# Optimization experiments

Measured on AMD Instinct MI355X. Metric: run time of the kernel, lower is better.

Reference implementation:

```python
import jax, jax.numpy as jnp
import numpy as np

VOCAB, XS, HS, NCLASS = 32000, 256, 256, 2
B, DEPTH = 128, 9
NTREE = 2 ** (DEPTH + 1) - 1  # 1023 nodes per perfect binary tree


def setup_inputs() -> dict:
    key = jax.random.key(0)
    ks = jax.random.split(key, 10)
    return {
        'types1': jax.random.randint(ks[0], (B, NTREE), 0, VOCAB, dtype=jnp.int32),
        'types2': jax.random.randint(ks[1], (B, NTREE), 0, VOCAB, dtype=jnp.int32),
        'emb': jax.random.normal(ks[2], (VOCAB, XS), jnp.float32) * 0.1,
        'W_iou': jax.random.normal(ks[3], (3 * HS, XS), jnp.float32) * 0.05,
        'U_iou': jax.random.normal(ks[4], (3 * HS, HS), jnp.float32) * 0.05,
        'b_iou': jnp.zeros((1, 3 * HS), jnp.float32),
        'U_f_w': jax.random.normal(ks[5], (HS, HS), jnp.float32) * 0.05,
        'U_f_b': jnp.zeros((HS,), jnp.float32),
        'cls_w': jax.random.normal(ks[6], (NCLASS, HS), jnp.float32) * 0.05,
        'cls_b': jnp.zeros((NCLASS,), jnp.float32),
    }


def _tree_forward(types, emb, W_iou, U_iou, b_iou, U_f_w, U_f_b):
    # types: [B, NTREE] heap layout (node j has children 2j+1, 2j+2)
    x = emb[types]                       # [B, N, XS] embedding gather
    wx = x @ W_iou.T                     # [B, N, 3H] leaf iou (DGL reduce overwrites it for internal nodes)
    h = jnp.zeros((types.shape[0], NTREE, HS), wx.dtype)
    c = jnp.zeros_like(h)
    for lvl in range(DEPTH, -1, -1):     # bottom-up topological levels (static)
        idx = np.arange(2 ** lvl - 1, 2 ** (lvl + 1) - 1)
        if lvl == DEPTH:  # leaves: no mailbox, keep W_iou(x)
            iou = wx[:, idx] + b_iou
            c_sum = 0.0
        else:
            ch = np.stack([2 * idx + 1, 2 * idx + 2], axis=-1)  # [n, 2]
            h_ch = h[:, ch]              # [B, n, 2, H] child mailbox
            c_ch = c[:, ch]
            h_tild = h_ch.sum(axis=2)
            f = jax.nn.sigmoid(h_ch @ U_f_w.T + U_f_b)
            c_sum = (f * c_ch).sum(axis=2)
            iou = h_tild @ U_iou.T + b_iou  # overwrites wx per DGL semantics
        i, o, u = jnp.split(iou, 3, axis=-1)
        c_new = jax.nn.sigmoid(i) * jnp.tanh(u) + c_sum
        h_new = jax.nn.sigmoid(o) * jnp.tanh(c_new)
        h = h.at[:, idx].set(h_new)
        c = c.at[:, idx].set(c_new)
    return h.mean(axis=1)                # AvgPooling over nodes -> [B, H]


def reference(types1, types2, emb, W_iou, U_iou, b_iou, U_f_w, U_f_b, cls_w, cls_b):
    rep1 = _tree_forward(types1, emb, W_iou, U_iou, b_iou, U_f_w, U_f_b)
    rep2 = _tree_forward(types2, emb, W_iou, U_iou, b_iou, U_f_w, U_f_b)
    return jnp.abs(rep1 - rep2) @ cls_w.T + cls_b  # [B, NCLASS]
```

## Files before the change

kernel.cpp:

```cpp
#include <hip/hip_runtime.h>
#include <math.h>


typedef _Float16 h16;
typedef h16 f16x8 __attribute__((ext_vector_type(8)));
typedef h16 h16x4 __attribute__((ext_vector_type(4)));
typedef float f32x4 __attribute__((ext_vector_type(4)));

#define HS 256
#define NTREE 1023
#define B2 256

#define DMA16(gp, lp) __builtin_amdgcn_global_load_lds( \
    (const __attribute__((address_space(1))) void*)(gp), \
    (__attribute__((address_space(3))) void*)(lp), 16, 0, 0)

__device__ __forceinline__ float sigf(float x){
  return __builtin_amdgcn_rcpf(1.0f + exp2f(x * -1.44269504f));
}
__device__ __forceinline__ float sig_mul_tanh(float a, float b){
  const float E1 = exp2f(a * -1.44269504f);
  const float E2 = exp2f(fminf(b * -2.88539008f, 126.0f));
  return (1.0f - E2) * __builtin_amdgcn_rcpf((1.0f + E1) * (1.0f + E2));
}

__global__ __launch_bounds__(256) void convert_all(const float* __restrict__ emb,
    const float* __restrict__ Ufw, const float* __restrict__ Uiou,
    const float* __restrict__ Wiou, h16* __restrict__ emb16,
    h16* __restrict__ W16, h16* __restrict__ Wx16, float* __restrict__ rep){
  if (blockIdx.x < 64)
    ((float4*)rep)[blockIdx.x*256 + threadIdx.x] = make_float4(0.f,0.f,0.f,0.f);
  const size_t i0 = ((size_t)blockIdx.x*256 + threadIdx.x)*8;
  const float* src; h16* dst; size_t off;
  if (i0 < 8192000UL){ src = emb;  dst = emb16;       off = i0; }
  else if (i0 < 8257536UL){ src = Ufw;  dst = W16;        off = i0 - 8192000UL; }
  else if (i0 < 8454144UL){ src = Uiou; dst = W16+65536;  off = i0 - 8257536UL; }
  else               { src = Wiou; dst = Wx16;       off = i0 - 8454144UL; }
  const float4 v0 = *(const float4*)&src[off];
  const float4 v1 = *(const float4*)&src[off+4];
  f16x8 o;
  o[0]=(h16)v0.x; o[1]=(h16)v0.y; o[2]=(h16)v0.z; o[3]=(h16)v0.w;
  o[4]=(h16)v1.x; o[5]=(h16)v1.y; o[6]=(h16)v1.z; o[7]=(h16)v1.w;
  *(f16x8*)&dst[off] = o;
}

__global__ __launch_bounds__(256) void swizzle_all(const h16* __restrict__ W16,
    const h16* __restrict__ Wx16, h16* __restrict__ Wfrag,
    h16* __restrict__ WxFrag){
  const int tid = blockIdx.x*256 + threadIdx.x;
  if (tid < 65536){
    const int lane = tid & 63;
    const int f    = (tid >> 6) & 15;
    const int kc   = (tid >> 10) & 7;
    const int cb   = tid >> 13;
    const int g = f >> 2, cf = f & 3;
    const int row = g*256 + cb*64 + cf*16 + (lane & 15);
    const int col = kc*32 + (lane >> 4)*8;
    const f16x8 v = *(const f16x8*)&W16[(size_t)row*256 + col];
    *(f16x8*)&Wfrag[(size_t)tid*8] = v;
  } else {
    const int t2 = tid - 65536;
    const int lane = t2 & 63;
    const int frag = t2 >> 6;
    const int cb  = frag / 96;
    const int rem = frag % 96;
    const int kc  = rem / 12;
    const int f   = rem % 12;
    const int g = f >> 2, cf = f & 3;
    const int row = g*256 + cb*64 + cf*16 + (lane & 15);
    const int col = kc*32 + (lane >> 4)*8;
    const f16x8 v = *(const f16x8*)&Wx16[(size_t)row*256 + col];
    *(f16x8*)&WxFrag[(size_t)frag*512 + lane*8] = v;
  }
}

__global__ __launch_bounds__(256,3) void ht_mfma(const h16* __restrict__ emb16,
    const h16* __restrict__ WxFrag, const float* __restrict__ biou,
    h16* __restrict__ hT, h16* __restrict__ cT){
  __shared__ h16 ldsA[4*8*64*8];
  __shared__ h16 ldsB[12*64*8];
  const int t = threadIdx.x, w = t >> 6, l = t & 63;
  const int q = l >> 4, li = l & 15;
  const int waveR = w & 1, waveC = w >> 1;
  const int bx = blockIdx.x;

  {
    const int grow = bx*64 + w*16 + li;
    const size_t abase = (size_t)grow * 256;
    #pragma unroll
    for (int kc=0; kc<8; ++kc)
      DMA16(emb16 + abase + kc*32 + q*8, &ldsA[(w*8 + kc)*512]);
  }

  for (int cb=0; cb<4; ++cb){
    const h16* wfBase = WxFrag + (size_t)cb*8*12*512 + (size_t)l*8;

    #pragma unroll
    for (int i=0; i<3; ++i)
      DMA16(wfBase + ((size_t)(w*3 + i))*512, &ldsB[(w*3 + i)*512]);
    __syncthreads();

    f32x4 acc[3][2][2] = {};
    #pragma unroll
    for (int kc=0; kc<8; ++kc){
      f16x8 aF[2], bF[3][2];
      #pragma unroll
      for (int rt=0; rt<2; ++rt)
        aF[rt] = *(const f16x8*)&ldsA[(((waveR*2 + rt)*8 + kc)*64 + l)*8];
      #pragma unroll
      for (int g=0; g<3; ++g)
        #pragma unroll
        for (int ct=0; ct<2; ++ct)
          bF[g][ct] = *(const f16x8*)&ldsB[((g*4 + waveC*2 + ct)*64 + l)*8];
      __syncthreads();
      if (kc < 7){
        #pragma unroll
        for (int i=0; i<3; ++i)
          DMA16(wfBase + ((size_t)(kc+1)*12 + w*3 + i)*512,
                &ldsB[(w*3 + i)*512]);
      }
      #pragma unroll
      for (int g=0; g<3; ++g)
        #pragma unroll
        for (int rt=0; rt<2; ++rt)
          #pragma unroll
          for (int ct=0; ct<2; ++ct)
            acc[g][rt][ct] = __builtin_amdgcn_mfma_f32_16x16x32_f16(
                aF[rt], bF[g][ct], acc[g][rt][ct], 0,0,0);
      __syncthreads();
    }

    #pragma unroll
    for (int ct=0; ct<2; ++ct){
      const int c = cb*64 + waveC*32 + ct*16 + li;
      const float bi = biou[c], bo = biou[256+c], bu = biou[512+c];
      #pragma unroll
      for (int rt=0; rt<2; ++rt){
        #pragma unroll
        for (int reg=0; reg<4; ++reg){
          const int row = bx*64 + waveR*32 + rt*16 + q*4 + reg;
          const float iv = acc[0][rt][ct][reg] + bi;
          const float ov = acc[1][rt][ct][reg] + bo;
          const float uv = acc[2][rt][ct][reg] + bu;
          const float cc = sig_mul_tanh(iv, uv);
          const float hh = sig_mul_tanh(ov, cc);
          hT[(size_t)row*256 + c] = (h16)hh;
          cT[(size_t)row*256 + c] = (h16)cc;
        }
      }
    }
  }
}

__global__ __launch_bounds__(256,3) void gt16_mfma(const h16* __restrict__ hT,
    const h16* __restrict__ Wfrag, const float* __restrict__ biou,
    const float* __restrict__ Ufb, h16* __restrict__ GT16){
  __shared__ h16 ldsA[4*8*64*8];
  __shared__ h16 ldsB[16*64*8];
  const int t = threadIdx.x, w = t >> 6, l = t & 63;
  const int q = l >> 4, li = l & 15;
  const int waveR = w & 1, waveC = w >> 1;
  const int bx = blockIdx.x;

  {
    const int grow = bx*64 + w*16 + li;
    const size_t abase = (size_t)grow * 256;
    #pragma unroll
    for (int kc=0; kc<8; ++kc)
      DMA16(hT + abase + kc*32 + q*8, &ldsA[(w*8 + kc)*512]);
  }

  for (int cb=0; cb<4; ++cb){
    const h16* wfBase = Wfrag + (size_t)cb*8*16*512 + (size_t)l*8;

    #pragma unroll
    for (int i=0; i<4; ++i)
      DMA16(wfBase + ((size_t)(w*4 + i))*512, &ldsB[(w*4 + i)*512]);
    __syncthreads();

    f32x4 acc[4][2][2] = {};
    #pragma unroll
    for (int kc=0; kc<8; ++kc){
      f16x8 aF[2], bF[4][2];
      #pragma unroll
      for (int rt=0; rt<2; ++rt)
        aF[rt] = *(const f16x8*)&ldsA[(((waveR*2 + rt)*8 + kc)*64 + l)*8];
      #pragma unroll
      for (int g=0; g<4; ++g)
        #pragma unroll
        for (int ct=0; ct<2; ++ct)
          bF[g][ct] = *(const f16x8*)&ldsB[((g*4 + waveC*2 + ct)*64 + l)*8];
      __syncthreads();
      if (kc < 7){
        #pragma unroll
        for (int i=0; i<4; ++i)
          DMA16(wfBase + ((size_t)(kc+1)*16 + w*4 + i)*512,
                &ldsB[(w*4 + i)*512]);
      }
      #pragma unroll
      for (int g=0; g<4; ++g)
        #pragma unroll
        for (int rt=0; rt<2; ++rt)
          #pragma unroll
          for (int ct=0; ct<2; ++ct)
            acc[g][rt][ct] = __builtin_amdgcn_mfma_f32_16x16x32_f16(
                aF[rt], bF[g][ct], acc[g][rt][ct], 0,0,0);
      __syncthreads();
    }

    #pragma unroll
    for (int ct=0; ct<2; ++ct){
      const int c = cb*64 + waveC*32 + ct*16 + li;
      const float fb  = Ufb[c];
      const float bi2 = 0.5f*biou[c], bo2 = 0.5f*biou[256+c], bu2 = 0.5f*biou[512+c];
      #pragma unroll
      for (int rt=0; rt<2; ++rt){
        #pragma unroll
        for (int reg=0; reg<4; ++reg){
          const int row = bx*64 + waveR*32 + rt*16 + q*4 + reg;
          h16x4 o;
          o[0] = (h16)(acc[0][rt][ct][reg] + fb);
          o[1] = (h16)(acc[1][rt][ct][reg] + bi2);
          o[2] = (h16)(acc[2][rt][ct][reg] + bo2);
          o[3] = (h16)(acc[3][rt][ct][reg] + bu2);
          *(h16x4*)&GT16[(size_t)row*1024 + c*4] = o;
        }
      }
    }
  }
}

__global__ __launch_bounds__(256) void lvl8_cell(const int* __restrict__ t1,
    const int* __restrict__ t2, const h16* __restrict__ GT16,
    const h16* __restrict__ cT, const h16* __restrict__ hT,
    h16* __restrict__ hUpHigh, h16* __restrict__ cPar,
    float* __restrict__ rep){
  const int k = threadIdx.x;
  const int m0 = blockIdx.x*32;
  const int rr = m0 >> 8;
  const int* tp = (rr < 128) ? t1 : t2;
  const int b = rr & 127;
  float s = 0.f;
  #pragma unroll 4
  for (int p=0; p<32; ++p){
    const int m = m0 + p, jn = m & 255;
    const size_t vl = (size_t)tp[b*NTREE + 511 + 2*jn];
    const size_t vr = (size_t)tp[b*NTREE + 512 + 2*jn];
    const h16x4 gl = *(const h16x4*)&GT16[vl*1024 + k*4];
    const h16x4 gr = *(const h16x4*)&GT16[vr*1024 + k*4];
    const float cl = (float)cT[vl*256 + k];
    const float cr = (float)cT[vr*256 + k];
    const float fl = sigf((float)gl[0]);
    const float fr = sigf((float)gr[0]);
    const float iv = (float)gl[1] + (float)gr[1];
    const float ov = (float)gl[2] + (float)gr[2];
    const float uv = (float)gl[3] + (float)gr[3];
    const float cnew = sig_mul_tanh(iv, uv) + fl*cl + fr*cr;
    const float hnew = sig_mul_tanh(ov, cnew);
    hUpHigh[((size_t)jn*256 + rr)*256 + k] = (h16)hnew;
    cPar[(size_t)m*256 + k] = (h16)cnew;
    s += (float)hT[vl*256 + k] + (float)hT[vr*256 + k];
  }
  atomicAdd(&rep[rr*HS + k], s);
}

__global__ __launch_bounds__(256,3) void level_mfma(
    const h16* __restrict__ hChild, const h16* __restrict__ cChild,
    const h16* __restrict__ Wfrag,
    const float* __restrict__ biou, const float* __restrict__ Ufb,
    h16* __restrict__ hUpW, h16* __restrict__ cPar,
    int log2n, int cbN, int cOff, int ndOff){
  const int n = 1 << log2n;
  const int mask2 = 2*n - 1;
  __shared__ h16 ldsA[4*8*64*8];
  __shared__ h16 ldsB[16*64*8];
  const int t = threadIdx.x, w = t >> 6, l = t & 63;
  const int q = l >> 4, li = l & 15;
  const int waveR = w & 1, waveC = w >> 1;
  const int bx = blockIdx.x;

  {
    const int grow = bx*64 + w*16 + li;
    const int cidx = grow & mask2;
    const int rr   = grow >> (log2n + 1);
    const size_t abase = ((size_t)(cOff + cidx)*256 + rr)*256;
    #pragma unroll
    for (int kc=0; kc<8; ++kc)
      DMA16(hChild + abase + kc*32 + q*8, &ldsA[(w*8 + kc)*512]);
  }

  for (int cb=0; cb<cbN; ++cb){
    const int cbi = blockIdx.y*cbN + cb;
    const int colBase = cbi*64;
    const h16* wfBase = Wfrag + (size_t)cbi*8*16*512 + (size_t)l*8;

    #pragma unroll
    for (int i=0; i<4; ++i)
      DMA16(wfBase + ((size_t)(w*4 + i))*512, &ldsB[(w*4 + i)*512]);
    __syncthreads();

    f32x4 acc[4][2][2] = {};
    #pragma unroll
    for (int kc=0; kc<8; ++kc){
      f16x8 aF[2], bF[4][2];
      #pragma unroll
      for (int rt=0; rt<2; ++rt)
        aF[rt] = *(const f16x8*)&ldsA[(((waveR*2 + rt)*8 + kc)*64 + l)*8];
      #pragma unroll
      for (int g=0; g<4; ++g)
        #pragma unroll
        for (int ct=0; ct<2; ++ct)
          bF[g][ct] = *(const f16x8*)&ldsB[((g*4 + waveC*2 + ct)*64 + l)*8];
      __syncthreads();
      if (kc < 7){
        #pragma unroll
        for (int i=0; i<4; ++i)
          DMA16(wfBase + ((size_t)(kc+1)*16 + w*4 + i)*512,
                &ldsB[(w*4 + i)*512]);
      }
      #pragma unroll
      for (int g=0; g<4; ++g)
        #pragma unroll
        for (int rt=0; rt<2; ++rt)
          #pragma unroll
          for (int ct=0; ct<2; ++ct)
            acc[g][rt][ct] = __builtin_amdgcn_mfma_f32_16x16x32_f16(
                aF[rt], bF[g][ct], acc[g][rt][ct], 0,0,0);
      __syncthreads();
    }

    #pragma unroll
    for (int ct=0; ct<2; ++ct){
      const int c = colBase + waveC*32 + ct*16 + li;
      const float fb  = Ufb[c];
      const float bi_ = biou[c], bo_ = biou[256+c], bu_ = biou[512+c];
      #pragma unroll
      for (int rt=0; rt<2; ++rt){
        #pragma unroll
        for (int pp=0; pp<2; ++pp){
          const int crel = waveR*32 + rt*16 + q*4 + 2*pp;
          const int m = bx*32 + (crel >> 1);
          const int rr2 = m >> log2n;
          const int jn = m & (n - 1);
          const float cl = (float)cChild[(size_t)(bx*64 + crel)*256 + c];
          const float cr = (float)cChild[(size_t)(bx*64 + crel + 1)*256 + c];
          const float fl = sigf(acc[0][rt][ct][2*pp]   + fb);
          const float fr = sigf(acc[0][rt][ct][2*pp+1] + fb);
          const float iv = acc[1][rt][ct][2*pp] + acc[1][rt][ct][2*pp+1] + bi_;
          const float ov = acc[2][rt][ct][2*pp] + acc[2][rt][ct][2*pp+1] + bo_;
          const float uv = acc[3][rt][ct][2*pp] + acc[3][rt][ct][2*pp+1] + bu_;
          const float cnew = sig_mul_tanh(iv, uv) + fl*cl + fr*cr;
          const float hnew = sig_mul_tanh(ov, cnew);
          hUpW[(((size_t)(ndOff + jn))*256 + rr2)*256 + c] = (h16)hnew;
          cPar[((size_t)m)*256 + c] = (h16)cnew;
        }
      }
    }
  }
}

__global__ __launch_bounds__(256) void rep_accum(const h16* __restrict__ H,
    float* __restrict__ rep, int nrows, int chunk){
  const int r = blockIdx.y, k = threadIdx.x;
  const int n0 = blockIdx.x * chunk;
  int n1 = n0 + chunk; if (n1 > nrows) n1 = nrows;
  float s = 0.f;
  for (int nd = n0; nd < n1; ++nd)
    s += (float)H[((size_t)nd*256 + r)*HS + k];
  atomicAdd(&rep[r*HS + k], s);
}

__global__ __launch_bounds__(256) void cls_kernel(const float* __restrict__ rep,
    const float* __restrict__ clsw, const float* __restrict__ clsb,
    float* __restrict__ out){
  const int b = blockIdx.x, k = threadIdx.x;
  const float d = fabsf(rep[b*HS + k] - rep[(128+b)*HS + k]) * (1.0f/1023.0f);
  __shared__ float r0[256], r1[256];
  r0[k] = d * clsw[k];
  r1[k] = d * clsw[HS + k];
  __syncthreads();
  for (int off = 128; off > 0; off >>= 1){
    if (k < off){ r0[k] += r0[k+off]; r1[k] += r1[k+off]; }
    __syncthreads();
  }
  if (k == 0){
    out[b*2 + 0] = r0[0] + clsb[0];
    out[b*2 + 1] = r1[0] + clsb[1];
  }
}

extern "C" void kernel_launch(void* const* d_in, const int* in_sizes, int n_in,
                              void* d_out, int out_size, void* d_ws, size_t ws_size,
                              hipStream_t stream){
  const int*   types1 = (const int*)d_in[0];
  const int*   types2 = (const int*)d_in[1];
  const float* emb    = (const float*)d_in[2];
  const float* Wiou   = (const float*)d_in[3];
  const float* Uiou   = (const float*)d_in[4];
  const float* biou   = (const float*)d_in[5];
  const float* Ufw    = (const float*)d_in[6];
  const float* Ufb    = (const float*)d_in[7];
  const float* clsw   = (const float*)d_in[8];
  const float* clsb   = (const float*)d_in[9];
  float* out = (float*)d_out;

  h16* ws      = (h16*)d_ws;
  h16* GT16    = ws;
  h16* emb16   = ws + 24576000UL;
  h16* Wx16    = ws + 32768000UL;
  h16* hUpLow  = ws;
  h16* cB      = ws + 16711680UL;
  h16* hT      = ws + 65536000UL;
  h16* cT      = ws + 73728000UL;
  h16* hUpHigh = ws + 81920000UL;
  h16* cA      = ws + 98697216UL;
  h16* W16     = ws + 115474432UL;
  h16* Wfrag   = ws + 115736576UL;
  float* rep   = (float*)(ws + 116260864UL);
  h16* WxFrag  = ws + 116391936UL;

  convert_all<<<4224, 256, 0, stream>>>(emb, Ufw, Uiou, Wiou, emb16, W16, Wx16, rep);
  swizzle_all<<<352, 256, 0, stream>>>(W16, Wx16, Wfrag, WxFrag);
  ht_mfma<<<500, 256, 0, stream>>>(emb16, WxFrag, biou, hT, cT);
  gt16_mfma<<<500, 256, 0, stream>>>(hT, Wfrag, biou, Ufb, GT16);
  lvl8_cell<<<2048, 256, 0, stream>>>(types1, types2, GT16, cT, hT,
                                      hUpHigh, cA, rep);

  const h16* cprev = cA;
  for (int lvl = 7; lvl >= 0; --lvl){
    const int children = 512 << lvl;
    const int cbN = (lvl == 7) ? 2 : ((lvl == 6) ? 4 : 1);
    h16* cout = ((8 - lvl) & 1) ? cB : cA;
    const h16* hin = (lvl == 7) ? hUpHigh : hUpLow;
    const int cOff  = (lvl == 7) ? 0 : ((1 << (lvl + 1)) - 1);
    const int ndOff = (1 << lvl) - 1;
    level_mfma<<<dim3(children/64, 4/cbN), 256, 0, stream>>>(
        hin, cprev, Wfrag, biou, Ufb, hUpLow, cout,
        lvl, cbN, cOff, ndOff);
    cprev = cout;
  }
  rep_accum<<<dim3(2, B2), 256, 0, stream>>>(hUpLow,  rep, 255, 128);
  rep_accum<<<dim3(2, B2), 256, 0, stream>>>(hUpHigh, rep, 256, 128);
  cls_kernel<<<128, 256, 0, stream>>>(rep, clsw, clsb, out);
}
```

Measured before the change: 449.5 us.

## Fuse top six tree levels into one per-tree kernel with LDS-resident state

Replaces the per-level launches for levels 5 through 0 with a single tree_tail kernel in which each block owns one tree and keeps its h and c state in LDS across levels. Per-node hidden sums are accumulated into the pooled representation inside the kernel, so rep_accum only covers the lower nodes. Levels 7 and 6 are now launched with a fixed 4-way column split. This removes several small launches and global round trips for the narrow top levels, at the cost of low parallelism (256 blocks, one per tree) and heavy LDS use.

```diff
diff --git a/kernel.cpp b/kernel.cpp
--- a/kernel.cpp
+++ b/kernel.cpp
@@ -359,6 +359,137 @@
   }
 }
 
+template<int RT, int N>
+__device__ __forceinline__ void tail_level(const h16* Ain, h16* Aout,
+    const h16* Cin, h16* Cout, const h16* __restrict__ Wfrag,
+    const float* __restrict__ biou, const float* __restrict__ Ufb,
+    float* ldsRep, h16* Bs,
+    int t, int w, int l, int q, int li, int waveR, int waveC){
+  constexpr int rtCnt = (RT == 4) ? 2 : 1;
+  for (int cb=0; cb<4; ++cb){
+    const h16* wfBase = Wfrag + (size_t)cb*65536 + (size_t)l*8;
+    #pragma unroll
+    for (int i=0; i<4; ++i)
+      DMA16(wfBase + ((size_t)(w*4 + i))*512, &Bs[(w*4 + i)*512]);
+    __syncthreads();
+
+    f32x4 acc[4][2][2] = {};
+    for (int kc=0; kc<8; ++kc){
+      f16x8 aF[2], bF[4][2];
+      #pragma unroll
+      for (int rt=0; rt<rtCnt; ++rt){
+        const int rti = (RT == 4) ? (waveR*2 + rt) : ((RT == 2) ? waveR : 0);
+        aF[rt] = *(const f16x8*)&Ain[((rti*8 + kc)*64 + l)*8];
+      }
+      #pragma unroll
+      for (int g=0; g<4; ++g)
+        #pragma unroll
+        for (int ct=0; ct<2; ++ct)
+          bF[g][ct] = *(const f16x8*)&Bs[((g*4 + waveC*2 + ct)*64 + l)*8];
+      __syncthreads();
+      if (kc < 7){
+        #pragma unroll
+        for (int i=0; i<4; ++i)
+          DMA16(wfBase + ((size_t)(kc+1)*16 + w*4 + i)*512,
+                &Bs[(w*4 + i)*512]);
+      }
+      #pragma unroll
+      for (int g=0; g<4; ++g)
+        #pragma unroll
+        for (int rt=0; rt<rtCnt; ++rt)
+          #pragma unroll
+          for (int ct=0; ct<2; ++ct)
+            acc[g][rt][ct] = __builtin_amdgcn_mfma_f32_16x16x32_f16(
+                aF[rt], bF[g][ct], acc[g][rt][ct], 0,0,0);
+      __syncthreads();
+    }
+
+    #pragma unroll
+    for (int ct=0; ct<2; ++ct){
+      const int c = cb*64 + waveC*32 + ct*16 + li;
+      const float fb  = Ufb[c];
+      const float bi_ = biou[c], bo_ = biou[256+c], bu_ = biou[512+c];
+      float repPart = 0.f;
+      #pragma unroll
+      for (int rt=0; rt<rtCnt; ++rt){
+        #pragma unroll
+        for (int pp=0; pp<2; ++pp){
+          const int crel = ((RT == 4) ? (waveR*32 + rt*16)
+                           : (RT == 2) ? (waveR*16) : 0) + q*4 + 2*pp;
+          const int pr = crel >> 1;
+          const bool valid = (pr < N) && !(RT == 1 && waveR == 1);
+          const float cl = (float)Cin[crel*256 + c];
+          const float cr = (float)Cin[(crel+1)*256 + c];
+          const float fl = sigf(acc[0][rt][ct][2*pp]   + fb);
+          const float fr = sigf(acc[0][rt][ct][2*pp+1] + fb);
+          const float iv = acc[1][rt][ct][2*pp] + acc[1][rt][ct][2*pp+1] + bi_;
+          const float ov = acc[2][rt][ct][2*pp] + acc[2][rt][ct][2*pp+1] + bo_;
+          const float uv = acc[3][rt][ct][2*pp] + acc[3][rt][ct][2*pp+1] + bu_;
+          const float cnew = sig_mul_tanh(iv, uv) + fl*cl + fr*cr;
+          const float hnew = sig_mul_tanh(ov, cnew);
+          if (valid){
+            const int kc2 = c >> 5, qq = (c >> 3) & 3, j = c & 7;
+            const int tile = pr >> 4, li2 = pr & 15;
+            Aout[((tile*8 + kc2)*64 + qq*16 + li2)*8 + j] = (h16)hnew;
+            Cout[pr*256 + c] = (h16)cnew;
+            repPart += hnew;
+          }
+        }
+      }
+      atomicAdd(&ldsRep[c], repPart);
+    }
+  }
+  if (N < 16){
+    for (int pr=N; pr<16; ++pr){
+      const int c2 = t;
+      const int kc2 = c2 >> 5, qq = (c2 >> 3) & 3, j = c2 & 7;
+      Aout[((0*8 + kc2)*64 + qq*16 + (pr & 15))*8 + j] = (h16)0.f;
+    }
+  }
+}
+
+__global__ __launch_bounds__(256,1) void tree_tail(
+    const h16* __restrict__ hUpLow, const h16* __restrict__ cIn,
+    const h16* __restrict__ Wfrag, const float* __restrict__ biou,
+    const float* __restrict__ Ufb, float* __restrict__ rep){
+  __shared__ h16 A0[4*8*64*8];
+  __shared__ h16 A1[2*8*64*8];
+  __shared__ h16 Bs[16*64*8];
+  __shared__ h16 C0[64*256];
+  __shared__ h16 C1[32*256];
+  __shared__ float ldsRep[256];
+  const int t = threadIdx.x, w = t >> 6, l = t & 63;
+  const int q = l >> 4, li = l & 15;
+  const int waveR = w & 1, waveC = w >> 1;
+  const int rr = blockIdx.x;
+
+  ldsRep[t] = 0.f;
+
+  {
+    const int jj = w*16 + li;
+    const size_t abase = ((size_t)(63 + jj)*256 + rr)*256;
+    #pragma unroll
+    for (int kc=0; kc<8; ++kc)
+      DMA16(hUpLow + abase + kc*32 + q*8, &A0[(w*8 + kc)*512]);
+  }
+  {
+    const h16* src = cIn + (size_t)rr*16384 + (size_t)l*8;
+    #pragma unroll
+    for (int r2=0; r2<8; ++r2)
+      DMA16(src + ((size_t)(r2*4 + w))*512, &C0[(r2*4 + w)*512]);
+  }
+
+  tail_level<4,32>(A0, A1, C0, C1, Wfrag, biou, Ufb, ldsRep, Bs, t,w,l,q,li,waveR,waveC);
+  tail_level<2,16>(A1, A0, C1, C0, Wfrag, biou, Ufb, ldsRep, Bs, t,w,l,q,li,waveR,waveC);
+  tail_level<1,8> (A0, A1, C0, C1, Wfrag, biou, Ufb, ldsRep, Bs, t,w,l,q,li,waveR,waveC);
+  tail_level<1,4> (A1, A0, C1, C0, Wfrag, biou, Ufb, ldsRep, Bs, t,w,l,q,li,waveR,waveC);
+  tail_level<1,2> (A0, A1, C0, C1, Wfrag, biou, Ufb, ldsRep, Bs, t,w,l,q,li,waveR,waveC);
+  tail_level<1,1> (A1, A0, C1, C0, Wfrag, biou, Ufb, ldsRep, Bs, t,w,l,q,li,waveR,waveC);
+
+  __syncthreads();
+  atomicAdd(&rep[rr*HS + t], ldsRep[t]);
+}
+
 __global__ __launch_bounds__(256) void rep_accum(const h16* __restrict__ H,
     float* __restrict__ rep, int nrows, int chunk){
   const int r = blockIdx.y, k = threadIdx.x;
@@ -426,20 +557,13 @@
   lvl8_cell<<<2048, 256, 0, stream>>>(types1, types2, GT16, cT, hT,
                                       hUpHigh, cA, rep);
 
-  const h16* cprev = cA;
-  for (int lvl = 7; lvl >= 0; --lvl){
-    const int children = 512 << lvl;
-    const int cbN = (lvl == 7) ? 2 : ((lvl == 6) ? 4 : 1);
-    h16* cout = ((8 - lvl) & 1) ? cB : cA;
-    const h16* hin = (lvl == 7) ? hUpHigh : hUpLow;
-    const int cOff  = (lvl == 7) ? 0 : ((1 << (lvl + 1)) - 1);
-    const int ndOff = (1 << lvl) - 1;
-    level_mfma<<<dim3(children/64, 4/cbN), 256, 0, stream>>>(
-        hin, cprev, Wfrag, biou, Ufb, hUpLow, cout,
-        lvl, cbN, cOff, ndOff);
-    cprev = cout;
-  }
-  rep_accum<<<dim3(2, B2), 256, 0, stream>>>(hUpLow,  rep, 255, 128);
+  level_mfma<<<dim3(1024, 1), 256, 0, stream>>>(
+      hUpHigh, cA, Wfrag, biou, Ufb, hUpLow, cB, 7, 4, 0, 127);
+  level_mfma<<<dim3(512, 1), 256, 0, stream>>>(
+      hUpLow, cB, Wfrag, biou, Ufb, hUpLow, cA, 6, 4, 127, 63);
+  tree_tail<<<256, 256, 0, stream>>>(hUpLow, cA, Wfrag, biou, Ufb, rep);
+
+  rep_accum<<<dim3(2, B2), 256, 0, stream>>>(hUpLow + 63UL*65536UL, rep, 192, 96);
   rep_accum<<<dim3(2, B2), 256, 0, stream>>>(hUpHigh, rep, 256, 128);
   cls_kernel<<<128, 256, 0, stream>>>(rep, clsw, clsb, out);
 }
```

Measured after the change: 488.0 us. 8.6% more time.
